# Optimization experiments

Measured on AMD Instinct MI355X. Metric: run time of the kernel, lower is better.

Reference implementation:

```python
import jax, jax.numpy as jnp
import numpy as np

# Fixed architecture constants (match init_kwargs)
L = 4        # num_layers
E = 4        # embed_dim (forced: embedding rows are 4-bit patch vectors)
H = 512      # hidden_dim
NH = 8       # num_heads
HD = H // NH # head_dim = 64
FF = 1024    # feedforward_dim
S = 1024     # seq_len (num patches)
B = 4        # batch
NT = 17      # num_tokens (16 patterns + mask token)
MRP = 32     # max_relative_positions
EPS = 1e-5


def _layernorm(x, g, b):
    m = x.mean(-1, keepdims=True)
    v = x.var(-1, keepdims=True)  # torch LayerNorm uses biased variance
    return (x - m) / jnp.sqrt(v + EPS) * g + b


def setup_inputs() -> dict:
    key = jax.random.key(0)
    ks = jax.random.split(key, 16)
    patches = jax.random.randint(ks[0], (B, S), 0, 16)
    mask = jax.random.bernoulli(ks[1], 0.15, (B, S))
    # Frozen embedding table: rows 0..15 = binary 4-vectors, row 16 = all 2s (mask token)
    pat = np.array([[a, b, c, d] for a in range(2) for b in range(2)
                    for c in range(2) for d in range(2)], dtype=np.float32)
    emb = np.zeros((NT, E), np.float32)
    emb[:16] = pat
    emb[16] = 2.0
    emb_table = jnp.array(emb)

    def gn(k, shape, s=0.02):
        return jax.random.normal(k, shape, jnp.float32) * s

    return {
        'patches': patches,
        'mask': mask,
        'emb_table': emb_table,
        'Wi': gn(ks[2], (L, E, H)), 'bi': jnp.zeros((L, H)),
        'Wqkv': gn(ks[3], (L, H, 3 * H)), 'bqkv': jnp.zeros((L, 3 * H)),
        'Wo': gn(ks[4], (L, H, E)), 'bo': jnp.zeros((L, E)),
        'g1': jnp.ones((L, H)), 'b1n': jnp.zeros((L, H)),
        'Wf1': gn(ks[5], (L, E, FF)), 'bf1': jnp.zeros((L, FF)),
        'Wf2': gn(ks[6], (L, FF, E)), 'bf2': jnp.zeros((L, E)),
        'g2': jnp.ones((L, E)), 'b2n': jnp.zeros((L, E)),
        'relemb': jax.random.normal(ks[7], (L, 2 * MRP - 1, HD), jnp.float32),
        'Wout': gn(ks[8], (E, NT)), 'bout': jnp.zeros((NT,)),
    }


def reference(patches, mask, emb_table, Wi, bi, Wqkv, bqkv, Wo, bo,
              g1, b1n, Wf1, bf1, Wf2, bf2, g2, b2n, relemb, Wout, bout):
    # Embedding lookup + mask-token substitution
    x = emb_table[patches]                                # (B,S,E)
    x = jnp.where(mask[..., None], emb_table[-1], x)

    r = jnp.arange(S)
    relpos = jnp.clip(r[:, None] - r[None, :] + MRP - 1, 0, 2 * MRP - 2)  # (S,S)
    # The original's nested-loop mask-build reduces exactly to:
    #   score[b,q,k] += -inf  iff  mask[b,k] and q != k
    neg = jnp.where(mask[:, None, :] & (r[:, None] != r[None, :]),
                    -jnp.inf, 0.0)                        # (B,S,S)

    scale = 1.0 / np.sqrt(HD)
    for l in range(L):
        bias = relemb[l].sum(-1)[relpos]                  # (S,S) rel-pos bias
        xp = x @ Wi[l] + bi[l]                            # (B,S,H)
        xn = _layernorm(xp, g1[l], b1n[l])
        qkv = (xn @ Wqkv[l] + bqkv[l]).reshape(B, S, 3, NH, HD)
        q, k, v = qkv[:, :, 0], qkv[:, :, 1], qkv[:, :, 2]
        sc = jnp.einsum('bqhd,bkhd->bhqk', q, k) * scale + bias + neg[:, None]
        p = jax.nn.softmax(sc, axis=-1)                   # (B,NH,S,S)
        ao = jnp.einsum('bhqk,bkhd->bqhd', p, v).reshape(B, S, H)
        x = x + ao @ Wo[l] + bo[l]                        # residual 1 (embed dim E)
        ff = jax.nn.relu(_layernorm(x, g2[l], b2n[l]) @ Wf1[l] + bf1[l]) @ Wf2[l] + bf2[l]
        x = x + ff                                        # residual 2
    return x @ Wout + bout                                # (B,S,NT) logits
```

## Files before the change

### kernel.cpp

```cpp
#include <hip/hip_runtime.h>
#include <hip/hip_bf16.h>
#include <math.h>

#define B_ 4
#define S_ 1024
#define H_ 512
#define NH_ 8
#define HD_ 64
#define FF_ 1024
#define E_ 4
#define L_ 4
#define NT_ 17
#define BS_ 4096
#define EPS_ 1e-5f
#define L2E_ 1.4426950408889634f
#define SCL_ 0.18033688011112042f
#define KSPLIT_ 4

typedef __attribute__((ext_vector_type(8))) short short8;
typedef __attribute__((ext_vector_type(16))) float f32x16;
typedef float float4u __attribute__((ext_vector_type(4), aligned(4)));

__device__ inline ushort bf16_rne(float f) {
  unsigned u = __builtin_bit_cast(unsigned, f);
  u += 0x7FFFu + ((u >> 16) & 1u);
  return (ushort)(u >> 16);
}
__device__ inline unsigned pk_bf16(float a, float b) {
  return (unsigned)bf16_rne(a) | ((unsigned)bf16_rne(b) << 16);
}
__device__ inline unsigned pk2(float a, float b) {
  unsigned ua = __builtin_bit_cast(unsigned, a) + 0x8000u;
  unsigned ub = __builtin_bit_cast(unsigned, b) + 0x8000u;
  return __builtin_amdgcn_perm(ub, ua, 0x07060302u);
}
__device__ inline float ubf2f(ushort u) {
  return __builtin_bit_cast(float, ((unsigned)u) << 16);
}


__global__ __launch_bounds__(256) void k_init(const int* __restrict__ patches,
                                              const int* __restrict__ mask,
                                              const float* __restrict__ emb,
                                              const float* __restrict__ relemb,
                                              float* __restrict__ x,
                                              float* __restrict__ T,
                                              float* __restrict__ negT) {
  int gid = blockIdx.x * 256 + threadIdx.x;
  if (gid < BS_) {
    int mk = mask[gid];
    int row = mk ? (NT_ - 1) : patches[gid];
    ((float4*)x)[gid] = ((const float4*)emb)[row];
    negT[gid] = mk ? -1e30f : 0.f;
  } else {
    int idx = gid - BS_;
    if (idx < L_ * 2112) {
      int l = idx / 2112, j = idx - l * 2112;
      int c = 1086 - j;
      c = c < 0 ? 0 : (c > 62 ? 62 : c);
      const float* src = relemb + (size_t)(l * 63 + c) * 64;
      float s = 0.f;
#pragma unroll
      for (int d = 0; d < 64; d++) s += src[d];
      T[idx] = s * L2E_;
    }
  }
}

__global__ __launch_bounds__(256) void k_cvtw(const float* __restrict__ W,
                                              ushort* __restrict__ Wt) {
  __shared__ ushort Tr[64][72];
  int l = blockIdx.z, k0 = blockIdx.y * 64, n0 = blockIdx.x * 64;
  int t = threadIdx.x;
  const float* src = W + (size_t)l * 512 * 1536;
  int row = t >> 4, c4 = (t & 15) * 4;
#pragma unroll
  for (int rr = 0; rr < 4; rr++) {
    int k = rr * 16 + row;
    float4 v = *(const float4*)(src + (size_t)(k0 + k) * 1536 + n0 + c4);
    Tr[c4 + 0][k] = bf16_rne(v.x);
    Tr[c4 + 1][k] = bf16_rne(v.y);
    Tr[c4 + 2][k] = bf16_rne(v.z);
    Tr[c4 + 3][k] = bf16_rne(v.w);
  }
  __syncthreads();
  int nrow = t >> 2, kc = (t & 3) * 16;
  ushort* dst = Wt + ((size_t)(l * 1536 + n0 + nrow)) * 512 + k0 + kc;
  *(uint4*)dst = *(uint4*)&Tr[nrow][kc];
  *(uint4*)(dst + 8) = *(uint4*)&Tr[nrow][kc + 8];
}

__global__ __launch_bounds__(256) void k_inln(const float* __restrict__ x,
                                              const float* __restrict__ Wi,
                                              const float* __restrict__ bi,
                                              const float* __restrict__ g1,
                                              const float* __restrict__ b1n,
                                              ushort* __restrict__ xnbf) {
  __shared__ float red_s[4], red_q[4];
  int tok = blockIdx.x;
  int t = threadIdx.x;
  float4 xr = ((const float4*)x)[tok];
  int j0 = 2 * t, j1 = 2 * t + 1;
  float xp0 = bi[j0] + xr.x * Wi[j0] + xr.y * Wi[H_ + j0] + xr.z * Wi[2 * H_ + j0] + xr.w * Wi[3 * H_ + j0];
  float xp1 = bi[j1] + xr.x * Wi[j1] + xr.y * Wi[H_ + j1] + xr.z * Wi[2 * H_ + j1] + xr.w * Wi[3 * H_ + j1];
  float s = xp0 + xp1;
  float q = xp0 * xp0 + xp1 * xp1;
#pragma unroll
  for (int o = 32; o > 0; o >>= 1) {
    s += __shfl_xor(s, o);
    q += __shfl_xor(q, o);
  }
  int wid = t >> 6;
  if ((t & 63) == 0) { red_s[wid] = s; red_q[wid] = q; }
  __syncthreads();
  s = red_s[0] + red_s[1] + red_s[2] + red_s[3];
  q = red_q[0] + red_q[1] + red_q[2] + red_q[3];
  float mean = s * (1.f / (float)H_);
  float var = q * (1.f / (float)H_) - mean * mean;
  float rs = rsqrtf(var + EPS_);
  float v0 = (xp0 - mean) * rs * g1[j0] + b1n[j0];
  float v1 = (xp1 - mean) * rs * g1[j1] + b1n[j1];
  ((unsigned*)xnbf)[tok * 256 + t] = pk_bf16(v0, v1);
}

__global__ __launch_bounds__(256, 2) void k_qkv(const ushort* __restrict__ A,
                                                const ushort* __restrict__ Wt,
                                                const float* __restrict__ bias,
                                                ushort* __restrict__ qf,
                                                ushort* __restrict__ kf,
                                                ushort* __restrict__ vf) {
  __shared__ ushort At[2][128][72];
  __shared__ ushort Bt[2][128][72];
  int t = threadIdx.x;
  int n0 = blockIdx.x * 128, m0 = blockIdx.y * 128;
  bool tr = (n0 < 1024);
  int w = t >> 6, lq = t & 31, hh = (t >> 5) & 1;
  int wm = (w & 1) * 64, wn = (w >> 1) * 64;
  f32x16 acc[2][2];
#pragma unroll
  for (int mt = 0; mt < 2; mt++)
#pragma unroll
    for (int nt = 0; nt < 2; nt++)
#pragma unroll
      for (int i = 0; i < 16; i++) acc[mt][nt][i] = 0.f;

  uint4 ar[4], br[4];

#define QLOADREGS(k0_)                                                         \
  {                                                                            \
    _Pragma("unroll") for (int j = 0; j < 4; j++) {                            \
      int idl = 256 * j + t;                                                   \
      int row = idl >> 3, u = idl & 7;                                         \
      ar[j] = *(const uint4*)(A + (size_t)(m0 + row) * 512 + (k0_) + u * 8);   \
      br[j] = *(const uint4*)(Wt + (size_t)(n0 + row) * 512 + (k0_) + u * 8);  \
    }                                                                          \
  }
#define QWRITELDS(buf_)                                                        \
  {                                                                            \
    _Pragma("unroll") for (int j = 0; j < 4; j++) {                            \
      int idl = 256 * j + t;                                                   \
      int row = idl >> 3, u = idl & 7;                                         \
      *(uint4*)&At[buf_][row][u * 8] = ar[j];                                  \
      *(uint4*)&Bt[buf_][row][u * 8] = br[j];                                  \
    }                                                                          \
  }

  QLOADREGS(0);
  QWRITELDS(0);
  __syncthreads();

  for (int it = 0; it < 8; it++) {
    int buf = it & 1;
    if (it < 7) { QLOADREGS((it + 1) * 64); }
#pragma unroll
    for (int kc = 0; kc < 4; kc++) {
      short8 af[2], bf[2];
#pragma unroll
      for (int mt = 0; mt < 2; mt++) af[mt] = *(const short8*)&At[buf][wm + mt * 32 + lq][kc * 16 + hh * 8];
#pragma unroll
      for (int nt = 0; nt < 2; nt++) bf[nt] = *(const short8*)&Bt[buf][wn + nt * 32 + lq][kc * 16 + hh * 8];
#pragma unroll
      for (int mt = 0; mt < 2; mt++)
#pragma unroll
        for (int nt = 0; nt < 2; nt++) {
          if (tr)
            acc[mt][nt] = __builtin_amdgcn_mfma_f32_32x32x16_bf16(bf[nt], af[mt], acc[mt][nt], 0, 0, 0);
          else
            acc[mt][nt] = __builtin_amdgcn_mfma_f32_32x32x16_bf16(af[mt], bf[nt], acc[mt][nt], 0, 0, 0);
        }
    }
    if (it < 7) {
      QWRITELDS(buf ^ 1);
      __syncthreads();
    }
  }
#undef QLOADREGS
#undef QWRITELDS

  if (tr) {
#pragma unroll
    for (int mt = 0; mt < 2; mt++) {
      int token = m0 + wm + mt * 32 + lq;
      int bb = token >> 10, sr = token & 1023;
      int qt = sr >> 5, lqp = sr & 31;
#pragma unroll
      for (int nt = 0; nt < 2; nt++) {
        int nn = n0 + wn + nt * 32;
        int nloc = (nn < 512) ? nn : nn - 512;
        ushort* dst = (nn < 512) ? qf : kf;
        int hd = nloc >> 6;
        int bh = bb * 8 + hd;
        size_t fragbase = ((size_t)(bh * 32 + qt)) * 4 * 512;
#pragma unroll
        for (int rg = 0; rg < 4; rg++) {
          int nbase = nn + rg * 8 + hh * 4;
          float4 bv = *(const float4*)(bias + nbase);
          float v0 = acc[mt][nt][rg * 4 + 0] + bv.x;
          float v1 = acc[mt][nt][rg * 4 + 1] + bv.y;
          float v2 = acc[mt][nt][rg * 4 + 2] + bv.z;
          float v3 = acc[mt][nt][rg * 4 + 3] + bv.w;
          int d0 = (nloc & 63) + rg * 8 + hh * 4;
          size_t addr = fragbase + (size_t)(d0 >> 4) * 512 +
                        (size_t)(((d0 >> 3) & 1) * 32 + lqp) * 8 + (d0 & 7);
          *(uint2*)(dst + addr) = make_uint2(pk_bf16(v0, v1), pk_bf16(v2, v3));
        }
      }
    }
  } else {
#pragma unroll
    for (int nt = 0; nt < 2; nt++) {
      int n = n0 + wn + nt * 32 + lq;
      int nloc = n - 1024;
      int hd = nloc >> 6, d = nloc & 63;
      float bb_ = bias[n];
#pragma unroll
      for (int mt = 0; mt < 2; mt++) {
#pragma unroll
        for (int rg = 0; rg < 4; rg++) {
          int tb = m0 + wm + mt * 32 + rg * 8 + hh * 4;
          int bb = tb >> 10, sr = tb & 1023;
          int bh = bb * 8 + hd;
          float v0 = acc[mt][nt][rg * 4 + 0] + bb_;
          float v1 = acc[mt][nt][rg * 4 + 1] + bb_;
          float v2 = acc[mt][nt][rg * 4 + 2] + bb_;
          float v3 = acc[mt][nt][rg * 4 + 3] + bb_;
          size_t addr = ((size_t)((bh * 2 + (d >> 5)) * 64 + (sr >> 4))) * 512 +
                        (size_t)(((sr >> 3) & 1) * 32 + (d & 31)) * 8 + (sr & 7);
          *(uint2*)(vf + addr) = make_uint2(pk_bf16(v0, v1), pk_bf16(v2, v3));
        }
      }
    }
  }
}

__global__ __launch_bounds__(256, 3) void k_attn(const ushort* __restrict__ qf,
                                                 const ushort* __restrict__ kf,
                                                 const ushort* __restrict__ vf,
                                                 const float* __restrict__ Tl,
                                                 const float* __restrict__ negT,
                                                 ushort* __restrict__ Opart,
                                                 float* __restrict__ lpart) {
  __shared__ char smem[4 * 32 * 72 * 2];
  ushort(*Pt)[72] = (ushort(*)[72])(smem) ;
  unsigned(*Tb)[33] = (unsigned(*)[33])(smem);
  int t = threadIdx.x;
  int w = t >> 6, lane = t & 63;
  int lq = lane & 31, hh = lane >> 5;
  int id = blockIdx.x;
  int bh = id & 31;
  int slot = id >> 5;
  int qtg = slot & 7, j = slot >> 3;
  int b = bh >> 3, head = bh & 7;
  int qt = qtg * 4 + w;
  int q = qt * 32 + lq;
  int kstart = j * 256;

  const ushort* qbase = qf + ((size_t)(bh * 32 + qt)) * 2048 + lane * 8;
  short8 Qf[4];
#pragma unroll
  for (int c = 0; c < 4; c++) Qf[c] = *(const short8*)(qbase + c * 512);

  float Tlo = Tl[1086];
  float Thi = Tl[1024];

  float l_run = 0.f;
  f32x16 Ot[2];
#pragma unroll
  for (int dt = 0; dt < 2; dt++)
#pragma unroll
    for (int i = 0; i < 16; i++) Ot[dt][i] = 0.f;

  for (int it = 0; it < 4; it++) {
    int k0 = kstart + it * 64;
    short8 Kb[2][4];
#pragma unroll
    for (int st = 0; st < 2; st++) {
      const ushort* kb = kf + ((size_t)(bh * 32 + (k0 >> 5) + st)) * 2048 + lane * 8;
#pragma unroll
      for (int c = 0; c < 4; c++) Kb[st][c] = *(const short8*)(kb + c * 512);
    }
    short8 Vb[2][4];
#pragma unroll
    for (int dt = 0; dt < 2; dt++) {
      const ushort* vb = vf + ((size_t)((bh * 2 + dt) * 64 + (k0 >> 4))) * 512 + lane * 8;
#pragma unroll
      for (int c = 0; c < 4; c++) Vb[dt][c] = *(const short8*)(vb + c * 512);
    }
    f32x16 sa[2];
#pragma unroll
    for (int st = 0; st < 2; st++) {
      f32x16 a;
#pragma unroll
      for (int i = 0; i < 16; i++) a[i] = 0.f;
#pragma unroll
      for (int c = 0; c < 4; c++)
        a = __builtin_amdgcn_mfma_f32_32x32x16_bf16(Kb[st][c], Qf[c], a, 0, 0, 0);
      sa[st] = a;
    }
#pragma unroll
    for (int st = 0; st < 2; st++) {
      int kt0 = k0 + st * 32;
      int delta = kt0 - qt * 32;
      if (delta >= 64 || delta <= -64) {
        float bconst = (delta >= 64) ? Tlo : Thi;
#pragma unroll
        for (int rg = 0; rg < 4; rg++) {
          int krun = kt0 + rg * 8 + hh * 4;
          float4 nv = *(const float4*)(negT + b * S_ + krun);
          float p0 = exp2f(fmaf(sa[st][rg * 4 + 0], SCL_, bconst + nv.x));
          float p1 = exp2f(fmaf(sa[st][rg * 4 + 1], SCL_, bconst + nv.y));
          float p2 = exp2f(fmaf(sa[st][rg * 4 + 2], SCL_, bconst + nv.z));
          float p3 = exp2f(fmaf(sa[st][rg * 4 + 3], SCL_, bconst + nv.w));
          l_run += (p0 + p1) + (p2 + p3);
          *(uint2*)&Pt[w * 32 + lq][st * 32 + rg * 8 + hh * 4] = make_uint2(pk2(p0, p1), pk2(p2, p3));
        }
      } else {
#pragma unroll
        for (int rg = 0; rg < 4; rg++) {
          int krun = kt0 + rg * 8 + hh * 4;
          float4u bv = *(const float4u*)(Tl + (krun - q + 31 + 1024));
          float4 nv = *(const float4*)(negT + b * S_ + krun);
          float p[4];
#pragma unroll
          for (int i = 0; i < 4; i++) {
            float nvi = (i == 0) ? nv.x : (i == 1) ? nv.y : (i == 2) ? nv.z : nv.w;
            float t0 = (krun + i == q) ? bv[i] : (bv[i] + nvi);
            p[i] = exp2f(fmaf(sa[st][rg * 4 + i], SCL_, t0));
            l_run += p[i];
          }
          *(uint2*)&Pt[w * 32 + lq][st * 32 + rg * 8 + hh * 4] = make_uint2(pk2(p[0], p[1]), pk2(p[2], p[3]));
        }
      }
    }
    short8 Pf[4];
#pragma unroll
    for (int c = 0; c < 4; c++) Pf[c] = *(const short8*)&Pt[w * 32 + lq][c * 16 + hh * 8];
#pragma unroll
    for (int dt = 0; dt < 2; dt++)
#pragma unroll
      for (int c = 0; c < 4; c++)
        Ot[dt] = __builtin_amdgcn_mfma_f32_32x32x16_bf16(Vb[dt][c], Pf[c], Ot[dt], 0, 0, 0);
  }
  __syncthreads();
  unsigned(*tb)[33] = Tb + w * 32;
#pragma unroll
  for (int dt = 0; dt < 2; dt++)
#pragma unroll
    for (int rg = 0; rg < 4; rg++) {
      tb[lq][dt * 16 + rg * 4 + hh * 2 + 0] = pk2(Ot[dt][rg * 4 + 0], Ot[dt][rg * 4 + 1]);
      tb[lq][dt * 16 + rg * 4 + hh * 2 + 1] = pk2(Ot[dt][rg * 4 + 2], Ot[dt][rg * 4 + 3]);
    }
  __builtin_amdgcn_s_waitcnt(0);
#pragma unroll
  for (int s = 0; s < 16; s++) {
    int trow = s * 2 + hh;
    unsigned v = tb[trow][lq];
    unsigned* orow = (unsigned*)(Opart + (size_t)j * (BS_ * H_) +
                                 ((size_t)(b * S_ + qt * 32 + trow)) * H_ + head * 64);
    orow[lq] = v;
  }
  float l_tot = l_run + __shfl_xor(l_run, 32);
  if (hh == 0) lpart[((size_t)j * 32 + bh) * S_ + q] = l_tot;
}

__global__ __launch_bounds__(256) void k_resffn(const ushort* __restrict__ Opart,
                                                const float* __restrict__ lpart,
                                                const float* __restrict__ Wo,
                                                const float* __restrict__ bo,
                                                const float* __restrict__ g2,
                                                const float* __restrict__ b2n,
                                                const float* __restrict__ Wf1,
                                                const float* __restrict__ bf1,
                                                const float* __restrict__ Wf2,
                                                const float* __restrict__ bf2,
                                                float* __restrict__ x,
                                                const float* __restrict__ Wi,
                                                const float* __restrict__ bi,
                                                const float* __restrict__ g1,
                                                const float* __restrict__ b1n,
                                                ushort* __restrict__ xnbf,
                                                int doinln,
                                                const float* __restrict__ Wout,
                                                const float* __restrict__ bout,
                                                float* __restrict__ out,
                                                int dofinal) {
  int tok = blockIdx.x * 4 + (threadIdx.x >> 6);
  int lane = threadIdx.x & 63;
  int b = tok >> 10, qq = tok & 1023;
  const ushort* aor = Opart + (size_t)tok * H_;
  float r0 = 0, r1 = 0, r2 = 0, r3 = 0;
#pragma unroll
  for (int k = 0; k < H_ / 64; k++) {
    int kk = lane + k * 64;
    int lidx = (b * 8 + k) * 1024 + qq;
    float ls = lpart[lidx] + lpart[lidx + 32768] + lpart[lidx + 65536] + lpart[lidx + 98304];
    float a = ubf2f(aor[kk]) + ubf2f(aor[kk + 2097152]) +
              ubf2f(aor[kk + 2 * 2097152]) + ubf2f(aor[kk + 3 * 2097152]);
    a *= (1.f / ls);
    float4 w = *(const float4*)&Wo[kk * 4];
    r0 += a * w.x; r1 += a * w.y; r2 += a * w.z; r3 += a * w.w;
  }
#pragma unroll
  for (int o = 1; o < 64; o <<= 1) {
    r0 += __shfl_xor(r0, o); r1 += __shfl_xor(r1, o);
    r2 += __shfl_xor(r2, o); r3 += __shfl_xor(r3, o);
  }
  float4 xo = *(const float4*)&x[tok * 4];
  float x0 = xo.x + r0 + bo[0];
  float x1 = xo.y + r1 + bo[1];
  float x2 = xo.z + r2 + bo[2];
  float x3 = xo.w + r3 + bo[3];
  float mn = 0.25f * (x0 + x1 + x2 + x3);
  float d0 = x0 - mn, d1 = x1 - mn, d2 = x2 - mn, d3 = x3 - mn;
  float var = 0.25f * (d0 * d0 + d1 * d1 + d2 * d2 + d3 * d3);
  float rs = rsqrtf(var + EPS_);
  float l0 = d0 * rs * g2[0] + b2n[0];
  float l1 = d1 * rs * g2[1] + b2n[1];
  float l2 = d2 * rs * g2[2] + b2n[2];
  float l3 = d3 * rs * g2[3] + b2n[3];
  float f0 = 0, f1 = 0, f2 = 0, f3 = 0;
#pragma unroll
  for (int f4 = 0; f4 < FF_ / 64; f4++) {
    int f = lane + f4 * 64;
    float hh = bf1[f] + l0 * Wf1[f] + l1 * Wf1[FF_ + f] + l2 * Wf1[2 * FF_ + f] + l3 * Wf1[3 * FF_ + f];
    hh = fmaxf(hh, 0.f);
    float4 w2 = *(const float4*)&Wf2[f * 4];
    f0 += hh * w2.x; f1 += hh * w2.y; f2 += hh * w2.z; f3 += hh * w2.w;
  }
#pragma unroll
  for (int o = 1; o < 64; o <<= 1) {
    f0 += __shfl_xor(f0, o); f1 += __shfl_xor(f1, o);
    f2 += __shfl_xor(f2, o); f3 += __shfl_xor(f3, o);
  }
  x0 += f0 + bf2[0]; x1 += f1 + bf2[1]; x2 += f2 + bf2[2]; x3 += f3 + bf2[3];
  if (dofinal) {
    if (lane < NT_)
      out[tok * NT_ + lane] = bout[lane] + x0 * Wout[lane] + x1 * Wout[NT_ + lane] +
                              x2 * Wout[2 * NT_ + lane] + x3 * Wout[3 * NT_ + lane];
    return;
  }
  if (lane == 0) *(float4*)&x[tok * 4] = make_float4(x0, x1, x2, x3);
  if (doinln) {
    float xp[8];
    float s = 0.f, qs = 0.f;
#pragma unroll
    for (int k = 0; k < 8; k++) {
      int jj = 64 * k + lane;
      float v = bi[jj] + x0 * Wi[jj] + x1 * Wi[H_ + jj] + x2 * Wi[2 * H_ + jj] + x3 * Wi[3 * H_ + jj];
      xp[k] = v;
      s += v;
      qs += v * v;
    }
#pragma unroll
    for (int o = 1; o < 64; o <<= 1) {
      s += __shfl_xor(s, o);
      qs += __shfl_xor(qs, o);
    }
    float mean = s * (1.f / (float)H_);
    float var1 = qs * (1.f / (float)H_) - mean * mean;
    float rs1 = rsqrtf(var1 + EPS_);
#pragma unroll
    for (int k = 0; k < 8; k++) {
      int jj = 64 * k + lane;
      float v = (xp[k] - mean) * rs1 * g1[jj] + b1n[jj];
      xnbf[tok * H_ + jj] = bf16_rne(v);
    }
  }
}

extern "C" void kernel_launch(void* const* d_in, const int* in_sizes, int n_in,
                              void* d_out, int out_size, void* d_ws, size_t ws_size,
                              hipStream_t stream) {
  const int* patches = (const int*)d_in[0];
  const int* mask = (const int*)d_in[1];
  const float* emb = (const float*)d_in[2];
  const float* Wi = (const float*)d_in[3];
  const float* bi = (const float*)d_in[4];
  const float* Wqkv = (const float*)d_in[5];
  const float* bqkv = (const float*)d_in[6];
  const float* Wo = (const float*)d_in[7];
  const float* bo = (const float*)d_in[8];
  const float* g1 = (const float*)d_in[9];
  const float* b1n = (const float*)d_in[10];
  const float* Wf1 = (const float*)d_in[11];
  const float* bf1 = (const float*)d_in[12];
  const float* Wf2 = (const float*)d_in[13];
  const float* bf2 = (const float*)d_in[14];
  const float* g2 = (const float*)d_in[15];
  const float* b2n = (const float*)d_in[16];
  const float* relemb = (const float*)d_in[17];
  const float* Wout = (const float*)d_in[18];
  const float* bout = (const float*)d_in[19];
  float* out = (float*)d_out;

  char* p = (char*)d_ws;
  float* x = (float*)p;          p += (size_t)BS_ * 4 * 4;
  float* T = (float*)p;          p += (size_t)L_ * 2112 * 4;
  float* negT = (float*)p;       p += (size_t)BS_ * 4;
  float* lpart = (float*)p;      p += (size_t)KSPLIT_ * 32 * 1024 * 4;
  ushort* Opart = (ushort*)p;    p += (size_t)KSPLIT_ * BS_ * H_ * 2;
  ushort* xnbf = (ushort*)p;     p += (size_t)BS_ * H_ * 2;
  ushort* Wt = (ushort*)p;       p += (size_t)L_ * 1536 * 512 * 2;
  ushort* qf = (ushort*)p;       p += (size_t)32 * 1024 * 64 * 2;
  ushort* kf = (ushort*)p;       p += (size_t)32 * 1024 * 64 * 2;
  ushort* vf = (ushort*)p;       p += (size_t)32 * 64 * 1024 * 2;

  k_init<<<dim3(49), dim3(256), 0, stream>>>(patches, mask, emb, relemb, x, T, negT);
  k_cvtw<<<dim3(24, 8, 4), dim3(256), 0, stream>>>(Wqkv, Wt);
  k_inln<<<dim3(BS_), dim3(256), 0, stream>>>(x, Wi, bi, g1, b1n, xnbf);
  for (int l = 0; l < L_; l++) {
    k_qkv<<<dim3(12, 32), dim3(256), 0, stream>>>(xnbf, Wt + (size_t)l * 1536 * 512,
                                                  bqkv + l * 3 * H_, qf, kf, vf);
    k_attn<<<dim3(1024), dim3(256), 0, stream>>>(qf, kf, vf, T + l * 2112,
                                                 negT, Opart, lpart);
    int nl = l + 1;
    k_resffn<<<dim3(1024), dim3(256), 0, stream>>>(
        Opart, lpart, Wo + l * H_ * E_, bo + l * E_, g2 + l * E_, b2n + l * E_,
        Wf1 + l * E_ * FF_, bf1 + l * FF_, Wf2 + l * FF_ * E_, bf2 + l * E_, x,
        Wi + nl * E_ * H_, bi + nl * H_, g1 + nl * H_, b1n + nl * H_, xnbf,
        (l < L_ - 1) ? 1 : 0, Wout, bout, out, (l == L_ - 1) ? 1 : 0);
  }
}
```

Before: 340.5 us.

## Fuse Wo projection into attention epilogue with atomic split-K accumulation

The attention kernel now multiplies its unnormalized output tile by the head's slice of Wo (512->4) and atomically accumulates a per-head 4-float result and the softmax denominator, instead of writing bf16 partial O tiles for each key split. Key splits go from 4 to 8, so the grid doubles, and the QKV kernel zeroes the accumulation buffers. This removes the large Opart write and re-read in the residual/FFN kernel. The cost is float atomics, which make summation order nondeterministic, plus the zeroing pass.

New measurement: 481.2 us. 1.41x slower.

```diff
diff --git a/kernel.cpp b/kernel.cpp
--- a/kernel.cpp
+++ b/kernel.cpp
@@ -15,7 +15,7 @@
 #define EPS_ 1e-5f
 #define L2E_ 1.4426950408889634f
 #define SCL_ 0.18033688011112042f
-#define KSPLIT_ 4
+#define KSPLIT_ 8
 
 typedef __attribute__((ext_vector_type(8))) short short8;
 typedef __attribute__((ext_vector_type(16))) float f32x16;
@@ -128,11 +128,17 @@
                                                 const float* __restrict__ bias,
                                                 ushort* __restrict__ qf,
                                                 ushort* __restrict__ kf,
-                                                ushort* __restrict__ vf) {
+                                                ushort* __restrict__ vf,
+                                                float* __restrict__ AOz) {
   __shared__ ushort At[2][128][72];
   __shared__ ushort Bt[2][128][72];
   int t = threadIdx.x;
   int n0 = blockIdx.x * 128, m0 = blockIdx.y * 128;
+  {
+    int bid = blockIdx.y * 12 + blockIdx.x;
+    for (size_t idx = (size_t)bid * 256 + t; idx < 163840; idx += 384 * 256)
+      AOz[idx] = 0.f;
+  }
   bool tr = (n0 < 1024);
   int w = t >> 6, lq = t & 31, hh = (t >> 5) & 1;
   int wm = (w & 1) * 64, wn = (w >> 1) * 64;
@@ -258,11 +264,10 @@
                                                  const ushort* __restrict__ vf,
                                                  const float* __restrict__ Tl,
                                                  const float* __restrict__ negT,
-                                                 ushort* __restrict__ Opart,
-                                                 float* __restrict__ lpart) {
-  __shared__ char smem[4 * 32 * 72 * 2];
-  ushort(*Pt)[72] = (ushort(*)[72])(smem) ;
-  unsigned(*Tb)[33] = (unsigned(*)[33])(smem);
+                                                 const float* __restrict__ Wol,
+                                                 float* __restrict__ AO,
+                                                 float* __restrict__ L) {
+  __shared__ ushort Pt[4][32][72];
   int t = threadIdx.x;
   int w = t >> 6, lane = t & 63;
   int lq = lane & 31, hh = lane >> 5;
@@ -273,7 +278,7 @@
   int b = bh >> 3, head = bh & 7;
   int qt = qtg * 4 + w;
   int q = qt * 32 + lq;
-  int kstart = j * 256;
+  int kstart = j * 128;
 
   const ushort* qbase = qf + ((size_t)(bh * 32 + qt)) * 2048 + lane * 8;
   short8 Qf[4];
@@ -290,7 +295,7 @@
 #pragma unroll
     for (int i = 0; i < 16; i++) Ot[dt][i] = 0.f;
 
-  for (int it = 0; it < 4; it++) {
+  for (int it = 0; it < 2; it++) {
     int k0 = kstart + it * 64;
     short8 Kb[2][4];
 #pragma unroll
@@ -332,7 +337,7 @@
           float p2 = exp2f(fmaf(sa[st][rg * 4 + 2], SCL_, bconst + nv.z));
           float p3 = exp2f(fmaf(sa[st][rg * 4 + 3], SCL_, bconst + nv.w));
           l_run += (p0 + p1) + (p2 + p3);
-          *(uint2*)&Pt[w * 32 + lq][st * 32 + rg * 8 + hh * 4] = make_uint2(pk2(p0, p1), pk2(p2, p3));
+          *(uint2*)&Pt[w][lq][st * 32 + rg * 8 + hh * 4] = make_uint2(pk2(p0, p1), pk2(p2, p3));
         }
       } else {
 #pragma unroll
@@ -348,44 +353,52 @@
             p[i] = exp2f(fmaf(sa[st][rg * 4 + i], SCL_, t0));
             l_run += p[i];
           }
-          *(uint2*)&Pt[w * 32 + lq][st * 32 + rg * 8 + hh * 4] = make_uint2(pk2(p[0], p[1]), pk2(p[2], p[3]));
+          *(uint2*)&Pt[w][lq][st * 32 + rg * 8 + hh * 4] = make_uint2(pk2(p[0], p[1]), pk2(p[2], p[3]));
         }
       }
     }
     short8 Pf[4];
 #pragma unroll
-    for (int c = 0; c < 4; c++) Pf[c] = *(const short8*)&Pt[w * 32 + lq][c * 16 + hh * 8];
+    for (int c = 0; c < 4; c++) Pf[c] = *(const short8*)&Pt[w][lq][c * 16 + hh * 8];
 #pragma unroll
     for (int dt = 0; dt < 2; dt++)
 #pragma unroll
       for (int c = 0; c < 4; c++)
         Ot[dt] = __builtin_amdgcn_mfma_f32_32x32x16_bf16(Vb[dt][c], Pf[c], Ot[dt], 0, 0, 0);
   }
-  __syncthreads();
-  unsigned(*tb)[33] = Tb + w * 32;
+  const float* woh = Wol + head * 64 * 4;
+  float pe0 = 0.f, pe1 = 0.f, pe2 = 0.f, pe3 = 0.f;
 #pragma unroll
   for (int dt = 0; dt < 2; dt++)
 #pragma unroll
-    for (int rg = 0; rg < 4; rg++) {
-      tb[lq][dt * 16 + rg * 4 + hh * 2 + 0] = pk2(Ot[dt][rg * 4 + 0], Ot[dt][rg * 4 + 1]);
-      tb[lq][dt * 16 + rg * 4 + hh * 2 + 1] = pk2(Ot[dt][rg * 4 + 2], Ot[dt][rg * 4 + 3]);
-    }
-  __builtin_amdgcn_s_waitcnt(0);
-#pragma unroll
-  for (int s = 0; s < 16; s++) {
-    int trow = s * 2 + hh;
-    unsigned v = tb[trow][lq];
-    unsigned* orow = (unsigned*)(Opart + (size_t)j * (BS_ * H_) +
-                                 ((size_t)(b * S_ + qt * 32 + trow)) * H_ + head * 64);
-    orow[lq] = v;
-  }
+    for (int rg = 0; rg < 4; rg++)
+#pragma unroll
+      for (int i = 0; i < 4; i++) {
+        int d = dt * 32 + rg * 8 + hh * 4 + i;
+        float4 wv = *(const float4*)(woh + d * 4);
+        float o = Ot[dt][rg * 4 + i];
+        pe0 = fmaf(o, wv.x, pe0);
+        pe1 = fmaf(o, wv.y, pe1);
+        pe2 = fmaf(o, wv.z, pe2);
+        pe3 = fmaf(o, wv.w, pe3);
+      }
+  pe0 += __shfl_xor(pe0, 32);
+  pe1 += __shfl_xor(pe1, 32);
+  pe2 += __shfl_xor(pe2, 32);
+  pe3 += __shfl_xor(pe3, 32);
   float l_tot = l_run + __shfl_xor(l_run, 32);
-  if (hh == 0) lpart[((size_t)j * 32 + bh) * S_ + q] = l_tot;
-}
-
-__global__ __launch_bounds__(256) void k_resffn(const ushort* __restrict__ Opart,
-                                                const float* __restrict__ lpart,
-                                                const float* __restrict__ Wo,
+  if (hh == 0) {
+    float* ao = AO + ((size_t)(b * S_ + q) * NH_ + head) * 4;
+    atomicAdd(ao + 0, pe0);
+    atomicAdd(ao + 1, pe1);
+    atomicAdd(ao + 2, pe2);
+    atomicAdd(ao + 3, pe3);
+    atomicAdd(&L[bh * S_ + q], l_tot);
+  }
+}
+
+__global__ __launch_bounds__(256) void k_resffn(const float* __restrict__ AO,
+                                                const float* __restrict__ L,
                                                 const float* __restrict__ bo,
                                                 const float* __restrict__ g2,
                                                 const float* __restrict__ b2n,
@@ -407,21 +420,12 @@
   int tok = blockIdx.x * 4 + (threadIdx.x >> 6);
   int lane = threadIdx.x & 63;
   int b = tok >> 10, qq = tok & 1023;
-  const ushort* aor = Opart + (size_t)tok * H_;
-  float r0 = 0, r1 = 0, r2 = 0, r3 = 0;
-#pragma unroll
-  for (int k = 0; k < H_ / 64; k++) {
-    int kk = lane + k * 64;
-    int lidx = (b * 8 + k) * 1024 + qq;
-    float ls = lpart[lidx] + lpart[lidx + 32768] + lpart[lidx + 65536] + lpart[lidx + 98304];
-    float a = ubf2f(aor[kk]) + ubf2f(aor[kk + 2097152]) +
-              ubf2f(aor[kk + 2 * 2097152]) + ubf2f(aor[kk + 3 * 2097152]);
-    a *= (1.f / ls);
-    float4 w = *(const float4*)&Wo[kk * 4];
-    r0 += a * w.x; r1 += a * w.y; r2 += a * w.z; r3 += a * w.w;
-  }
-#pragma unroll
-  for (int o = 1; o < 64; o <<= 1) {
+  int h = lane & 7;
+  float inv = 1.f / L[(b * 8 + h) * 1024 + qq];
+  float4 v = *(const float4*)(AO + ((size_t)tok * 8 + h) * 4);
+  float r0 = v.x * inv, r1 = v.y * inv, r2 = v.z * inv, r3 = v.w * inv;
+#pragma unroll
+  for (int o = 1; o < 8; o <<= 1) {
     r0 += __shfl_xor(r0, o); r1 += __shfl_xor(r1, o);
     r2 += __shfl_xor(r2, o); r3 += __shfl_xor(r3, o);
   }
@@ -466,10 +470,10 @@
 #pragma unroll
     for (int k = 0; k < 8; k++) {
       int jj = 64 * k + lane;
-      float v = bi[jj] + x0 * Wi[jj] + x1 * Wi[H_ + jj] + x2 * Wi[2 * H_ + jj] + x3 * Wi[3 * H_ + jj];
-      xp[k] = v;
-      s += v;
-      qs += v * v;
+      float v2 = bi[jj] + x0 * Wi[jj] + x1 * Wi[H_ + jj] + x2 * Wi[2 * H_ + jj] + x3 * Wi[3 * H_ + jj];
+      xp[k] = v2;
+      s += v2;
+      qs += v2 * v2;
     }
 #pragma unroll
     for (int o = 1; o < 64; o <<= 1) {
@@ -482,8 +486,8 @@
 #pragma unroll
     for (int k = 0; k < 8; k++) {
       int jj = 64 * k + lane;
-      float v = (xp[k] - mean) * rs1 * g1[jj] + b1n[jj];
-      xnbf[tok * H_ + jj] = bf16_rne(v);
+      float v2 = (xp[k] - mean) * rs1 * g1[jj] + b1n[jj];
+      xnbf[tok * H_ + jj] = bf16_rne(v2);
     }
   }
 }
@@ -517,8 +521,8 @@
   float* x = (float*)p;          p += (size_t)BS_ * 4 * 4;
   float* T = (float*)p;          p += (size_t)L_ * 2112 * 4;
   float* negT = (float*)p;       p += (size_t)BS_ * 4;
-  float* lpart = (float*)p;      p += (size_t)KSPLIT_ * 32 * 1024 * 4;
-  ushort* Opart = (ushort*)p;    p += (size_t)KSPLIT_ * BS_ * H_ * 2;
+  float* AO = (float*)p;         p += (size_t)BS_ * NH_ * 4 * 4;
+  float* L = (float*)p;          p += (size_t)32 * 1024 * 4;
   ushort* xnbf = (ushort*)p;     p += (size_t)BS_ * H_ * 2;
   ushort* Wt = (ushort*)p;       p += (size_t)L_ * 1536 * 512 * 2;
   ushort* qf = (ushort*)p;       p += (size_t)32 * 1024 * 64 * 2;
@@ -530,12 +534,12 @@
   k_inln<<<dim3(BS_), dim3(256), 0, stream>>>(x, Wi, bi, g1, b1n, xnbf);
   for (int l = 0; l < L_; l++) {
     k_qkv<<<dim3(12, 32), dim3(256), 0, stream>>>(xnbf, Wt + (size_t)l * 1536 * 512,
-                                                  bqkv + l * 3 * H_, qf, kf, vf);
-    k_attn<<<dim3(1024), dim3(256), 0, stream>>>(qf, kf, vf, T + l * 2112,
-                                                 negT, Opart, lpart);
+                                                  bqkv + l * 3 * H_, qf, kf, vf, AO);
+    k_attn<<<dim3(2048), dim3(256), 0, stream>>>(qf, kf, vf, T + l * 2112, negT,
+                                                 Wo + l * H_ * E_, AO, L);
     int nl = l + 1;
     k_resffn<<<dim3(1024), dim3(256), 0, stream>>>(
-        Opart, lpart, Wo + l * H_ * E_, bo + l * E_, g2 + l * E_, b2n + l * E_,
+        AO, L, bo + l * E_, g2 + l * E_, b2n + l * E_,
         Wf1 + l * E_ * FF_, bf1 + l * FF_, Wf2 + l * FF_ * E_, bf2 + l * E_, x,
         Wi + nl * E_ * H_, bi + nl * H_, g1 + nl * H_, b1n + nl * H_, xnbf,
         (l < L_ - 1) ? 1 : 0, Wout, bout, out, (l == L_ - 1) ? 1 : 0);
```
